# Kernel tuning notes

Hardware: AMD Instinct MI355X
Metric: run time of the kernel (lower is better)

The kernel has to match this reference:

```python
import jax, jax.numpy as jnp
import numpy as np

XMIN, XMAX = -16.0, 16.0
ZMIN, ZMAX = -16.0, 16.0
SOFTCLIP_L = 5.0


def ref2mem(traj, Zs, Xs):
    # traj: (B, T, 2) cam (x, z) -> mem pixel coords
    x = (traj[..., 0] - XMIN) / ((XMAX - XMIN) / Xs) - 0.5
    z = (traj[..., 1] - ZMIN) / ((ZMAX - ZMIN) / Zs) - 0.5
    return x, z


def bilinear_sample2d(pm, x, z):
    # pm: (B, C, Z, X); x, z: (B, N) float coords -> (B, C, N)
    B, C, Zs, Xs = pm.shape
    x = jnp.clip(x, 0.0, Xs - 1.0)
    z = jnp.clip(z, 0.0, Zs - 1.0)
    x0 = jnp.floor(x).astype(jnp.int32)
    z0 = jnp.floor(z).astype(jnp.int32)
    x1 = jnp.minimum(x0 + 1, Xs - 1)
    z1 = jnp.minimum(z0 + 1, Zs - 1)
    wx = x - x0.astype(x.dtype)
    wz = z - z0.astype(z.dtype)
    pm_flat = pm.reshape(B, C, Zs * Xs)

    def gather(zi, xi):
        idx = (zi * Xs + xi)[:, None, :]  # (B,1,N)
        return jnp.take_along_axis(pm_flat, jnp.broadcast_to(idx, (B, C, idx.shape[-1])), axis=2)

    v00 = gather(z0, x0); v01 = gather(z0, x1)
    v10 = gather(z1, x0); v11 = gather(z1, x1)
    wx = wx[:, None, :]; wz = wz[:, None, :]
    return (v00 * (1 - wx) * (1 - wz) + v01 * wx * (1 - wz)
            + v10 * (1 - wx) * wz + v11 * wx * wz)


def gru_cell(x, h, W_ih, W_hh, b_ih, b_hh):
    gi = x @ W_ih.T + b_ih
    gh = h @ W_hh.T + b_hh
    i_r, i_z, i_n = jnp.split(gi, 3, axis=1)
    h_r, h_z, h_n = jnp.split(gh, 3, axis=1)
    r = jax.nn.sigmoid(i_r + h_r)
    z = jax.nn.sigmoid(i_z + h_z)
    n = jnp.tanh(i_n + r * h_n)
    return (1.0 - z) * n + z * h


def expm_softclip(sig_raw):
    B = sig_raw.shape[0]
    nrm = jnp.linalg.norm(sig_raw.reshape(B, -1), axis=1)
    denom = jax.nn.logsumexp(jnp.stack([nrm / SOFTCLIP_L, jnp.ones_like(nrm)], axis=-1), axis=-1)
    return sig_raw / denom[:, None, None]


def reference(feat_map, pred_map, noise, traj_past,
              W_ih, W_hh, b_ih, b_hh, past_W, past_b,
              W1, b1, W2, b2, W3, b3):
    B, C, Zf, Xf = feat_map.shape
    Zp, Xp = pred_map.shape[2], pred_map.shape[3]
    T_futu = noise.shape[1]
    H = W_hh.shape[1]
    eye2 = jnp.eye(2, dtype=feat_map.dtype)

    # static feature: max_pool2d k=8 s=8 + past encoding
    pooled = feat_map.reshape(B, C, Zf // 8, 8, Xf // 8, 8).max(axis=(3, 5)).reshape(B, -1)
    past_enc = traj_past.reshape(B, -1) @ past_W.T + past_b
    sta_feat = jnp.concatenate([pooled, past_enc], axis=1)  # (B, 2080)

    def step(carry, noise_t):
        hx, win = carry
        xm, zm = ref2mem(win, Zp, Xp)
        feats = bilinear_sample2d(pred_map, xm, zm).reshape(B, -1)  # (B, 3)
        dyn_feat = jnp.concatenate([feats, win.reshape(B, -1)], axis=1)  # (B, 9)
        hx = gru_cell(dyn_feat, hx, W_ih, W_hh, b_ih, b_hh)
        joint = jnp.concatenate([hx, sta_feat], axis=1)  # (B, 2112)
        h1 = jax.nn.leaky_relu(joint @ W1.T + b1)
        h2 = jax.nn.leaky_relu(h1 @ W2.T + b2)
        pred = h2 @ W3.T + b3  # (B, 6)
        mu = pred[:, :2]
        sig_raw = pred[:, 2:].reshape(B, 2, 2) + 1e-8 * eye2
        sig_raw = expm_softclip(sig_raw)
        sig = jnp.einsum('bij,bkj->bik', sig_raw, sig_raw)
        xdotdot = mu + jnp.sum(sig * noise_t[:, None, :], axis=1)
        x_next = 2.0 * win[:, -1] - win[:, -2] + xdotdot  # verlet, dt=1
        win = jnp.concatenate([win[:, 1:], x_next[:, None]], axis=1)
        return (hx, win), x_next

    hx0 = jnp.zeros((B, H), dtype=feat_map.dtype)
    (_, _), traj_futu = jax.lax.scan(step, (hx0, traj_past), jnp.swapaxes(noise, 0, 1))
    return jnp.swapaxes(traj_futu, 0, 1)  # (B, T_futu, 2)


def setup_inputs():
    key = jax.random.key(0)
    ks = jax.random.split(key, 16)
    B, C, Zf, Xf = 192, 32, 64, 64
    T_futu, T_past, H = 27, 3, 32
    d = {}
    d['feat_map'] = jax.random.normal(ks[0], (B, C, Zf, Xf), jnp.float32)
    d['pred_map'] = jax.random.normal(ks[1], (B, 1, Zf, Xf), jnp.float32)
    d['noise'] = jax.random.normal(ks[2], (B, T_futu, 2), jnp.float32)
    d['traj_past'] = jax.random.normal(ks[3], (B, T_past, 2), jnp.float32) * 4.0
    s = 0.05
    d['W_ih'] = jax.random.normal(ks[4], (3 * H, 9), jnp.float32) * s
    d['W_hh'] = jax.random.normal(ks[5], (3 * H, H), jnp.float32) * s
    d['b_ih'] = jnp.zeros((3 * H,), jnp.float32)
    d['b_hh'] = jnp.zeros((3 * H,), jnp.float32)
    d['past_W'] = jax.random.normal(ks[6], (32, T_past * 2), jnp.float32) * s
    d['past_b'] = jnp.zeros((32,), jnp.float32)
    d['W1'] = jax.random.normal(ks[7], (64, 2112), jnp.float32) * 0.02
    d['b1'] = jnp.zeros((64,), jnp.float32)
    d['W2'] = jax.random.normal(ks[8], (32, 64), jnp.float32) * s
    d['b2'] = jnp.zeros((32,), jnp.float32)
    d['W3'] = jax.random.normal(ks[9], (6, 32), jnp.float32) * s
    d['b3'] = jnp.zeros((6,), jnp.float32)
    return d
```

## Files before the change

kernel.cpp:

```cpp
#include <hip/hip_runtime.h>
#include <hip/hip_bf16.h>
#include <math.h>

typedef unsigned int u32;
typedef __fp16 f16x2 __attribute__((ext_vector_type(2)));
typedef u32 u32x4 __attribute__((ext_vector_type(4)));

#define NB    192
#define NC    32
#define TFUT  27
#define BLOB_F_OFF (NB * 64)

#if __has_builtin(__builtin_amdgcn_rcpf)
#define RCPF(x) __builtin_amdgcn_rcpf(x)
#else
#define RCPF(x) (1.0f / (x))
#endif
#if __has_builtin(__builtin_amdgcn_sqrtf)
#define SQRTF(x) __builtin_amdgcn_sqrtf(x)
#else
#define SQRTF(x) sqrtf(x)
#endif
#if __has_builtin(__builtin_amdgcn_exp2f)
#define EXP2F(x) __builtin_amdgcn_exp2f(x)
#else
#define EXP2F(x) exp2f(x)
#endif
#if __has_builtin(__builtin_amdgcn_logf)
#define LOG2F(x) __builtin_amdgcn_logf(x)
#else
#define LOG2F(x) log2f(x)
#endif

__device__ __forceinline__ u32 pk16(float lo, float hi) {
    auto v = __builtin_amdgcn_cvt_pkrtz(lo, hi);
    return __builtin_bit_cast(u32, v);
}
__device__ __forceinline__ float fdot2pk(u32 a, u32 b, float c) {
#if __has_builtin(__builtin_amdgcn_fdot2)
    return __builtin_amdgcn_fdot2(__builtin_bit_cast(f16x2, a),
                                  __builtin_bit_cast(f16x2, b), c, false);
#else
    f16x2 av = __builtin_bit_cast(f16x2, a), bv = __builtin_bit_cast(f16x2, b);
    return c + (float)av[0] * (float)bv[0] + (float)av[1] * (float)bv[1];
#endif
}
__device__ __forceinline__ u32 rdl(u32 v, int lane) {
    return (u32)__builtin_amdgcn_readlane((int)v, lane);
}
__device__ __forceinline__ float rdlf(float v, int lane) {
    return __int_as_float(__builtin_amdgcn_readlane(__float_as_int(v), lane));
}
__device__ __forceinline__ float dpp_xor1(float v) {
    return __int_as_float(__builtin_amdgcn_update_dpp(
        0, __float_as_int(v), 0xB1, 0xF, 0xF, true));
}
__device__ __forceinline__ float perm32hi(float v) {
    int x = __float_as_int(v), y = x;
    asm volatile("v_permlane32_swap_b32 %0, %1" : "+v"(x), "+v"(y));
    return __int_as_float(x);
}
__device__ __forceinline__ float sigmoid_f(float x) {
    return RCPF(1.0f + EXP2F(-1.4426950408889634f * x));
}
__device__ __forceinline__ float tanh_f(float x) {
    return __builtin_fmaf(2.0f, RCPF(1.0f + EXP2F(-2.8853900817779268f * x)), -1.0f);
}

__global__ __launch_bounds__(1024) void k_static(
    const float* __restrict__ feat,
    const float* __restrict__ traj_past,
    const float* __restrict__ past_W,
    const float* __restrict__ past_b,
    const float* __restrict__ W1,
    const float* __restrict__ b1,
    const float* __restrict__ W_ih,
    const float* __restrict__ W_hh,
    const float* __restrict__ b_ih,
    const float* __restrict__ b_hh,
    const float* __restrict__ W2,
    const float* __restrict__ b2,
    const float* __restrict__ W3,
    const float* __restrict__ b3,
    float* __restrict__ ws)
{
    const int b = blockIdx.x;
    const int t = threadIdx.x;

    if (b == NB) {
        if (t >= 64) return;
        const int l = t, m2 = l & 31;
        u32* blob = reinterpret_cast<u32*>(ws) + BLOB_F_OFF + (size_t)l * 128;
        #pragma unroll
        for (int k = 0; k < 9; ++k) {
            blob[k]     = __float_as_uint(W_ih[l * 9 + k]);
            blob[9 + k] = __float_as_uint(W_ih[(64 + m2) * 9 + k]);
        }
        #pragma unroll
        for (int j = 0; j < 16; ++j) {
            blob[18 + j] = pk16(W_hh[l * 32 + 2*j],          W_hh[l * 32 + 2*j + 1]);
            blob[34 + j] = pk16(W_hh[(64 + m2) * 32 + 2*j],  W_hh[(64 + m2) * 32 + 2*j + 1]);
            blob[50 + j] = pk16(W1[(size_t)l * 2112 + 2*j],  W1[(size_t)l * 2112 + 2*j + 1]);
        }
        #pragma unroll
        for (int j = 0; j < 32; ++j)
            blob[66 + j] = pk16(W2[m2 * 64 + 2*j], W2[m2 * 64 + 2*j + 1]);
        const int wr = (l < 6) ? l : 0;
        #pragma unroll
        for (int j = 0; j < 16; ++j)
            blob[98 + j] = pk16(W3[wr * 32 + 2*j], W3[wr * 32 + 2*j + 1]);
        blob[114] = __float_as_uint(b_ih[l]);
        blob[115] = __float_as_uint(b_hh[l]);
        blob[116] = __float_as_uint(b_ih[64 + m2]);
        blob[117] = __float_as_uint(b_hh[64 + m2]);
        blob[118] = __float_as_uint(b2[m2]);
        #pragma unroll
        for (int r = 0; r < 6; ++r) blob[119 + r] = __float_as_uint(b3[r]);
        blob[125] = blob[126] = blob[127] = 0u;
        return;
    }

    __shared__ __align__(16) float sta[2080];

    for (int it = 0; it < 2; ++it) {
        const int c    = it * 16 + (t >> 6);
        const int cell = t & 63;
        const int zi = cell >> 3, xi = cell & 7;
        const float* p = feat + ((size_t)b * NC + c) * 4096 + zi * 8 * 64 + xi * 8;
        float m = -3.402823466e38f;
        #pragma unroll
        for (int dz = 0; dz < 8; ++dz) {
            const float4 v0 = *reinterpret_cast<const float4*>(p + dz * 64);
            const float4 v1 = *reinterpret_cast<const float4*>(p + dz * 64 + 4);
            m = fmaxf(m, fmaxf(fmaxf(fmaxf(v0.x, v0.y), fmaxf(v0.z, v0.w)),
                               fmaxf(fmaxf(v1.x, v1.y), fmaxf(v1.z, v1.w))));
        }
        sta[c * 64 + cell] = m;
    }
    if (t < 32) {
        float acc = past_b[t];
        #pragma unroll
        for (int k = 0; k < 6; ++k) acc += past_W[t * 6 + k] * traj_past[b * 6 + k];
        sta[2048 + t] = acc;
    }
    __syncthreads();

    const int o = t >> 4, l = t & 15;
    const float* wrow = W1 + (size_t)o * 2112 + 32;
    float acc = 0.f;
    #pragma unroll 4
    for (int j = 0; j < 32; ++j) {
        const int k = j * 64 + l * 4;
        const float4 w = *reinterpret_cast<const float4*>(wrow + k);
        const float4 s = *reinterpret_cast<const float4*>(&sta[k]);
        acc += w.x * s.x + w.y * s.y + w.z * s.z + w.w * s.w;
    }
    if (l < 8) {
        const int k = 2048 + l * 4;
        const float4 w = *reinterpret_cast<const float4*>(wrow + k);
        const float4 s = *reinterpret_cast<const float4*>(&sta[k]);
        acc += w.x * s.x + w.y * s.y + w.z * s.z + w.w * s.w;
    }
    acc += __shfl_xor(acc, 1);
    acc += __shfl_xor(acc, 2);
    acc += __shfl_xor(acc, 4);
    acc += __shfl_xor(acc, 8);
    if (l == 0) ws[b * 64 + o] = b1[o] + acc;
}

__global__ __launch_bounds__(64, 1) void k_recur(
    const float* __restrict__ pred_map,
    const float* __restrict__ noise,
    const float* __restrict__ traj_past,
    const float* __restrict__ ws,
    float* __restrict__ out)
{
    __shared__ __align__(16) float pm[4096];

    const int b = blockIdx.x;
    const int l = threadIdx.x;

    {
        const float4* src = reinterpret_cast<const float4*>(pred_map + (size_t)b * 4096);
        float4* dst = reinterpret_cast<float4*>(pm);
        #pragma unroll
        for (int i = 0; i < 16; ++i) dst[l + i * 64] = src[l + i * 64];
    }
    const float nzreg = (l < TFUT * 2) ? noise[b * (TFUT * 2) + l] : 0.f;

    const u32* blob = reinterpret_cast<const u32*>(ws) + BLOB_F_OFF + (size_t)l * 128;
    u32x4 dv[32];
    #pragma unroll
    for (int j = 0; j < 32; ++j)
        dv[j] = reinterpret_cast<const u32x4*>(blob)[j];
#define DW(i) (dv[(i) >> 2][(i) & 3])
#define DF(i) __int_as_float((int)DW(i))

    const float sta1l = ws[b * 64 + l];

    float w[6];
    #pragma unroll
    for (int j = 0; j < 6; ++j) w[j] = traj_past[b * 6 + j];
    float hxp = 0.f;
    u32 hxpk[16];
    #pragma unroll
    for (int j = 0; j < 16; ++j) hxpk[j] = 0u;
    float Adot = 0.f, Cdot = 0.f;

    __syncthreads();

    auto bsamp = [&](float px, float pz) -> float {
        float x = (px + 16.0f) * 2.0f - 0.5f;
        float z = (pz + 16.0f) * 2.0f - 0.5f;
        x = fminf(fmaxf(x, 0.0f), 63.0f);
        z = fminf(fmaxf(z, 0.0f), 63.0f);
        const float xf = floorf(x), zf = floorf(z);
        const int x0 = (int)xf, z0 = (int)zf;
        const int x1 = min(x0 + 1, 63), z1 = min(z0 + 1, 63);
        const float wx = x - xf, wz = z - zf;
        const float v00 = pm[z0 * 64 + x0], v01 = pm[z0 * 64 + x1];
        const float v10 = pm[z1 * 64 + x0], v11 = pm[z1 * 64 + x1];
        return v00 * (1.f - wx) * (1.f - wz) + v01 * wx * (1.f - wz)
             + v10 * (1.f - wx) * wz        + v11 * wx * wz;
    };
    float sm0 = bsamp(w[0], w[1]);
    float sm1 = bsamp(w[2], w[3]);
    float sm2 = bsamp(w[4], w[5]);

    for (int ts = 0; ts < TFUT; ++ts) {
        float gi  = DF(114) + DF(3) * w[0] + DF(4) * w[1] + DF(5) * w[2]
                            + DF(6) * w[3] + DF(7) * w[4] + DF(8) * w[5];
        float gi2 = DF(116) + DF(12) * w[0] + DF(13) * w[1] + DF(14) * w[2]
                            + DF(15) * w[3] + DF(16) * w[4] + DF(17) * w[5];
        gi  += DF(0) * sm0 + DF(1) * sm1 + DF(2) * sm2;
        gi2 += DF(9) * sm0 + DF(10) * sm1 + DF(11) * sm2;

        const float gs = gi + DF(115) + Adot;
        const float sg = sigmoid_f(gs);
        const float zv = perm32hi(sg);
        const float nv = tanh_f(gi2 + sg * (DF(117) + Cdot));
        const float hn = (1.0f - zv) * nv + zv * hxp;
        hxp = hn;

        const u32 hpk = pk16(hn, dpp_xor1(hn));
        #pragma unroll
        for (int j = 0; j < 16; ++j) hxpk[j] = rdl(hpk, 2 * j);

        float D0 = 0.f, D1 = 0.f, D2 = 0.f, D3 = 0.f;
        #pragma unroll
        for (int j = 0; j < 16; j += 4) {
            D0 = fdot2pk(hxpk[j],   DW(50 + j),     D0);
            D1 = fdot2pk(hxpk[j+1], DW(50 + j + 1), D1);
            D2 = fdot2pk(hxpk[j+2], DW(50 + j + 2), D2);
            D3 = fdot2pk(hxpk[j+3], DW(50 + j + 3), D3);
        }
        const float h1a = sta1l + ((D0 + D1) + (D2 + D3));
        const float h1l = (h1a >= 0.f) ? h1a : 0.01f * h1a;

        const u32 h1p = pk16(h1l, dpp_xor1(h1l));
        u32 h1pk[32];
        #pragma unroll
        for (int j = 0; j < 32; ++j) h1pk[j] = rdl(h1p, 2 * j);

        float P0 = 0.f, P1 = 0.f, P2 = 0.f, P3 = 0.f;
        float P4 = 0.f, P5 = 0.f, P6 = 0.f, P7 = 0.f;
        #pragma unroll
        for (int j = 0; j < 32; j += 8) {
            P0 = fdot2pk(h1pk[j],   DW(66 + j),     P0);
            P1 = fdot2pk(h1pk[j+1], DW(66 + j + 1), P1);
            P2 = fdot2pk(h1pk[j+2], DW(66 + j + 2), P2);
            P3 = fdot2pk(h1pk[j+3], DW(66 + j + 3), P3);
            P4 = fdot2pk(h1pk[j+4], DW(66 + j + 4), P4);
            P5 = fdot2pk(h1pk[j+5], DW(66 + j + 5), P5);
            P6 = fdot2pk(h1pk[j+6], DW(66 + j + 6), P6);
            P7 = fdot2pk(h1pk[j+7], DW(66 + j + 7), P7);
        }
        const float h2a = DF(118) + (((P0 + P1) + (P2 + P3)) + ((P4 + P5) + (P6 + P7)));
        const float h2l = (h2a >= 0.f) ? h2a : 0.01f * h2a;

        const u32 h2p = pk16(h2l, dpp_xor1(h2l));
        u32 h2pk[16];
        #pragma unroll
        for (int j = 0; j < 16; ++j) h2pk[j] = rdl(h2p, 2 * j);

        float Q0 = 0.f, Q1 = 0.f, Q2 = 0.f, Q3 = 0.f;
        #pragma unroll
        for (int j = 0; j < 16; j += 4) {
            Q0 = fdot2pk(h2pk[j],   DW(98 + j),     Q0);
            Q1 = fdot2pk(h2pk[j+1], DW(98 + j + 1), Q1);
            Q2 = fdot2pk(h2pk[j+2], DW(98 + j + 2), Q2);
            Q3 = fdot2pk(h2pk[j+3], DW(98 + j + 3), Q3);
        }
        const float praw = (Q0 + Q1) + (Q2 + Q3);

        const float pv0 = rdlf(praw, 0) + DF(119);
        const float pv1 = rdlf(praw, 1) + DF(120);
        const float pv2 = rdlf(praw, 2) + DF(121);
        const float pv3 = rdlf(praw, 3) + DF(122);
        const float pv4 = rdlf(praw, 4) + DF(123);
        const float pv5 = rdlf(praw, 5) + DF(124);

        const float s00 = pv2 + 1e-8f, s01 = pv3;
        const float s10 = pv4,          s11 = pv5 + 1e-8f;
        const float p00 = s00 * s00 + s01 * s01;
        const float p01 = s00 * s10 + s01 * s11;
        const float p11 = s10 * s10 + s11 * s11;
        const float nrm = SQRTF(p00 + p11);
        const float arg = nrm * 0.2f;
        const float mmx = fmaxf(arg, 1.0f);
        const float dd  = fabsf(arg - 1.0f);
        const float den = mmx + 0.6931471805599453f *
                          LOG2F(1.0f + EXP2F(-1.4426950408889634f * dd));
        const float inv  = RCPF(den);
        const float inv2 = inv * inv;

        const float nnx = rdlf(nzreg, 2 * ts);
        const float nny = rdlf(nzreg, 2 * ts + 1);
        const float xd0 = pv0 + nnx * ((p00 + p01) * inv2);
        const float xd1 = pv1 + nny * ((p01 + p11) * inv2);
        const float nx0 = 2.0f * w[4] - w[2] + xd0;
        const float nx1 = 2.0f * w[5] - w[3] + xd1;

        if (l == 0) {
            float2 o; o.x = nx0; o.y = nx1;
            *reinterpret_cast<float2*>(out + ((size_t)b * TFUT + ts) * 2) = o;
        }

        w[0] = w[2]; w[1] = w[3];
        w[2] = w[4]; w[3] = w[5];
        w[4] = nx0;  w[5] = nx1;
        sm0 = sm1; sm1 = sm2;

        float v00, v01, v10, v11, wxs, wzs;
        {
            float x = (nx0 + 16.0f) * 2.0f - 0.5f;
            float z = (nx1 + 16.0f) * 2.0f - 0.5f;
            x = fminf(fmaxf(x, 0.0f), 63.0f);
            z = fminf(fmaxf(z, 0.0f), 63.0f);
            const float xf = floorf(x), zf = floorf(z);
            const int x0 = (int)xf, z0 = (int)zf;
            const int x1 = min(x0 + 1, 63), z1 = min(z0 + 1, 63);
            wxs = x - xf; wzs = z - zf;
            v00 = pm[z0 * 64 + x0]; v01 = pm[z0 * 64 + x1];
            v10 = pm[z1 * 64 + x0]; v11 = pm[z1 * 64 + x1];
        }

        {
            float A0 = 0.f, A1 = 0.f, A2 = 0.f, A3 = 0.f;
            float C0 = 0.f, C1 = 0.f, C2 = 0.f, C3 = 0.f;
            #pragma unroll
            for (int j = 0; j < 16; j += 4) {
                A0 = fdot2pk(hxpk[j],   DW(18 + j),     A0);
                A1 = fdot2pk(hxpk[j+1], DW(18 + j + 1), A1);
                A2 = fdot2pk(hxpk[j+2], DW(18 + j + 2), A2);
                A3 = fdot2pk(hxpk[j+3], DW(18 + j + 3), A3);
                C0 = fdot2pk(hxpk[j],   DW(34 + j),     C0);
                C1 = fdot2pk(hxpk[j+1], DW(34 + j + 1), C1);
                C2 = fdot2pk(hxpk[j+2], DW(34 + j + 2), C2);
                C3 = fdot2pk(hxpk[j+3], DW(34 + j + 3), C3);
            }
            Adot = (A0 + A1) + (A2 + A3);
            Cdot = (C0 + C1) + (C2 + C3);
        }

        sm2 = v00 * (1.f - wxs) * (1.f - wzs) + v01 * wxs * (1.f - wzs)
            + v10 * (1.f - wxs) * wzs        + v11 * wxs * wzs;
    }
#undef DW
#undef DF
}

extern "C" void kernel_launch(void* const* d_in, const int* in_sizes, int n_in,
                              void* d_out, int out_size, void* d_ws, size_t ws_size,
                              hipStream_t stream) {
    const float* feat      = (const float*)d_in[0];
    const float* pred_map  = (const float*)d_in[1];
    const float* noise     = (const float*)d_in[2];
    const float* traj_past = (const float*)d_in[3];
    const float* W_ih      = (const float*)d_in[4];
    const float* W_hh      = (const float*)d_in[5];
    const float* b_ih      = (const float*)d_in[6];
    const float* b_hh      = (const float*)d_in[7];
    const float* past_W    = (const float*)d_in[8];
    const float* past_b    = (const float*)d_in[9];
    const float* W1        = (const float*)d_in[10];
    const float* b1        = (const float*)d_in[11];
    const float* W2        = (const float*)d_in[12];
    const float* b2        = (const float*)d_in[13];
    const float* W3        = (const float*)d_in[14];
    const float* b3        = (const float*)d_in[15];
    float* outp = (float*)d_out;
    float* ws   = (float*)d_ws;

    k_static<<<dim3(NB + 1), dim3(1024), 0, stream>>>(
        feat, traj_past, past_W, past_b, W1, b1,
        W_ih, W_hh, b_ih, b_hh, W2, b2, W3, b3, ws);
    k_recur<<<dim3(NB), dim3(64), 0, stream>>>(pred_map, noise, traj_past, ws, outp);
}
```

Before: 45.91 us.

## Broadcast recurrent vectors through LDS and split MLP dot products across half-waves

The per-step broadcasts of packed hidden vectors now go through small shared-memory buffers read back with vector loads, replacing long chains of readlane instructions. The W2 and W3 dot products are split so each half-wave covers half the inputs, and the halves are combined with a permlane32 swap, which shrinks the register weight blob. The A and C GRU dot products are moved earlier in the step to overlap with the MLP chain, and the bilinear sample uses lerp form. This relies on single-wave execution and only a compiler fence for LDS ordering, which is fragile. The perm32hi return value was also changed.

```diff
diff --git a/kernel.cpp b/kernel.cpp
--- a/kernel.cpp
+++ b/kernel.cpp
@@ -32,6 +32,8 @@
 #define LOG2F(x) log2f(x)
 #endif
 
+#define LDS_FENCE() asm volatile("" ::: "memory")
+
 __device__ __forceinline__ u32 pk16(float lo, float hi) {
     auto v = __builtin_amdgcn_cvt_pkrtz(lo, hi);
     return __builtin_bit_cast(u32, v);
@@ -45,9 +47,6 @@
     return c + (float)av[0] * (float)bv[0] + (float)av[1] * (float)bv[1];
 #endif
 }
-__device__ __forceinline__ u32 rdl(u32 v, int lane) {
-    return (u32)__builtin_amdgcn_readlane((int)v, lane);
-}
 __device__ __forceinline__ float rdlf(float v, int lane) {
     return __int_as_float(__builtin_amdgcn_readlane(__float_as_int(v), lane));
 }
@@ -58,7 +57,7 @@
 __device__ __forceinline__ float perm32hi(float v) {
     int x = __float_as_int(v), y = x;
     asm volatile("v_permlane32_swap_b32 %0, %1" : "+v"(x), "+v"(y));
-    return __int_as_float(x);
+    return __int_as_float(y);
 }
 __device__ __forceinline__ float sigmoid_f(float x) {
     return RCPF(1.0f + EXP2F(-1.4426950408889634f * x));
@@ -89,7 +88,7 @@
 
     if (b == NB) {
         if (t >= 64) return;
-        const int l = t, m2 = l & 31;
+        const int l = t, m2 = l & 31, h = l >> 5;
         u32* blob = reinterpret_cast<u32*>(ws) + BLOB_F_OFF + (size_t)l * 128;
         #pragma unroll
         for (int k = 0; k < 9; ++k) {
@@ -103,20 +102,20 @@
             blob[50 + j] = pk16(W1[(size_t)l * 2112 + 2*j],  W1[(size_t)l * 2112 + 2*j + 1]);
         }
         #pragma unroll
-        for (int j = 0; j < 32; ++j)
-            blob[66 + j] = pk16(W2[m2 * 64 + 2*j], W2[m2 * 64 + 2*j + 1]);
-        const int wr = (l < 6) ? l : 0;
-        #pragma unroll
         for (int j = 0; j < 16; ++j)
-            blob[98 + j] = pk16(W3[wr * 32 + 2*j], W3[wr * 32 + 2*j + 1]);
-        blob[114] = __float_as_uint(b_ih[l]);
-        blob[115] = __float_as_uint(b_hh[l]);
-        blob[116] = __float_as_uint(b_ih[64 + m2]);
-        blob[117] = __float_as_uint(b_hh[64 + m2]);
-        blob[118] = __float_as_uint(b2[m2]);
-        #pragma unroll
-        for (int r = 0; r < 6; ++r) blob[119 + r] = __float_as_uint(b3[r]);
-        blob[125] = blob[126] = blob[127] = 0u;
+            blob[66 + j] = pk16(W2[m2 * 64 + h * 32 + 2*j], W2[m2 * 64 + h * 32 + 2*j + 1]);
+        const int wr = (m2 < 6) ? m2 : 0;
+        #pragma unroll
+        for (int j = 0; j < 8; ++j)
+            blob[82 + j] = pk16(W3[wr * 32 + h * 16 + 2*j], W3[wr * 32 + h * 16 + 2*j + 1]);
+        blob[90] = __float_as_uint(b_ih[l]);
+        blob[91] = __float_as_uint(b_hh[l]);
+        blob[92] = __float_as_uint(b_ih[64 + m2]);
+        blob[93] = __float_as_uint(b_hh[64 + m2]);
+        blob[94] = __float_as_uint(b2[m2]);
+        #pragma unroll
+        for (int r = 0; r < 6; ++r) blob[95 + r] = __float_as_uint(b3[r]);
+        blob[101] = blob[102] = blob[103] = 0u;
         return;
     }
 
@@ -176,9 +175,14 @@
     float* __restrict__ out)
 {
     __shared__ __align__(16) float pm[4096];
+    __shared__ __align__(16) u32 hxbw[32];
+    __shared__ __align__(16) u32 h1bw[32];
+    __shared__ __align__(16) u32 h2bw[32];
 
     const int b = blockIdx.x;
     const int l = threadIdx.x;
+    const int h = l >> 5;
+    const bool odd = (l & 1);
 
     {
         const float4* src = reinterpret_cast<const float4*>(pred_map + (size_t)b * 4096);
@@ -189,9 +193,9 @@
     const float nzreg = (l < TFUT * 2) ? noise[b * (TFUT * 2) + l] : 0.f;
 
     const u32* blob = reinterpret_cast<const u32*>(ws) + BLOB_F_OFF + (size_t)l * 128;
-    u32x4 dv[32];
+    u32x4 dv[26];
     #pragma unroll
-    for (int j = 0; j < 32; ++j)
+    for (int j = 0; j < 26; ++j)
         dv[j] = reinterpret_cast<const u32x4*>(blob)[j];
 #define DW(i) (dv[(i) >> 2][(i) & 3])
 #define DF(i) __int_as_float((int)DW(i))
@@ -202,16 +206,13 @@
     #pragma unroll
     for (int j = 0; j < 6; ++j) w[j] = traj_past[b * 6 + j];
     float hxp = 0.f;
-    u32 hxpk[16];
-    #pragma unroll
-    for (int j = 0; j < 16; ++j) hxpk[j] = 0u;
     float Adot = 0.f, Cdot = 0.f;
 
     __syncthreads();
 
     auto bsamp = [&](float px, float pz) -> float {
-        float x = (px + 16.0f) * 2.0f - 0.5f;
-        float z = (pz + 16.0f) * 2.0f - 0.5f;
+        float x = __builtin_fmaf(2.0f, px, 31.5f);
+        float z = __builtin_fmaf(2.0f, pz, 31.5f);
         x = fminf(fmaxf(x, 0.0f), 63.0f);
         z = fminf(fmaxf(z, 0.0f), 63.0f);
         const float xf = floorf(x), zf = floorf(z);
@@ -220,85 +221,140 @@
         const float wx = x - xf, wz = z - zf;
         const float v00 = pm[z0 * 64 + x0], v01 = pm[z0 * 64 + x1];
         const float v10 = pm[z1 * 64 + x0], v11 = pm[z1 * 64 + x1];
-        return v00 * (1.f - wx) * (1.f - wz) + v01 * wx * (1.f - wz)
-             + v10 * (1.f - wx) * wz        + v11 * wx * wz;
+        const float top = v00 + wx * (v01 - v00);
+        const float bot = v10 + wx * (v11 - v10);
+        return top + wz * (bot - top);
     };
     float sm0 = bsamp(w[0], w[1]);
     float sm1 = bsamp(w[2], w[3]);
     float sm2 = bsamp(w[4], w[5]);
 
+    auto pkpair = [&](float v) -> u32 {
+        const float nb = dpp_xor1(v);
+        const float plo = odd ? nb : v;
+        const float phi = odd ? v : nb;
+        return pk16(plo, phi);
+    };
+
     for (int ts = 0; ts < TFUT; ++ts) {
-        float gi  = DF(114) + DF(3) * w[0] + DF(4) * w[1] + DF(5) * w[2]
-                            + DF(6) * w[3] + DF(7) * w[4] + DF(8) * w[5];
-        float gi2 = DF(116) + DF(12) * w[0] + DF(13) * w[1] + DF(14) * w[2]
-                            + DF(15) * w[3] + DF(16) * w[4] + DF(17) * w[5];
-        gi  += DF(0) * sm0 + DF(1) * sm1 + DF(2) * sm2;
-        gi2 += DF(9) * sm0 + DF(10) * sm1 + DF(11) * sm2;
-
-        const float gs = gi + DF(115) + Adot;
+        float giA = DF(90) + DF(3) * w[0] + DF(4) * w[1];
+        float giB = DF(5) * w[2] + DF(6) * w[3];
+        float giC = DF(7) * w[4] + DF(8) * w[5];
+        float giD = DF(0) * sm0 + DF(1) * sm1 + DF(2) * sm2;
+        const float gi = (giA + giB) + (giC + giD);
+
+        float gjA = DF(92) + DF(12) * w[0] + DF(13) * w[1];
+        float gjB = DF(14) * w[2] + DF(15) * w[3];
+        float gjC = DF(16) * w[4] + DF(17) * w[5];
+        float gjD = DF(9) * sm0 + DF(10) * sm1 + DF(11) * sm2;
+        const float gi2 = (gjA + gjB) + (gjC + gjD);
+
+        const float gs = gi + DF(91) + Adot;
         const float sg = sigmoid_f(gs);
         const float zv = perm32hi(sg);
-        const float nv = tanh_f(gi2 + sg * (DF(117) + Cdot));
+        const float nv = tanh_f(gi2 + sg * (DF(93) + Cdot));
         const float hn = (1.0f - zv) * nv + zv * hxp;
         hxp = hn;
 
-        const u32 hpk = pk16(hn, dpp_xor1(hn));
-        #pragma unroll
-        for (int j = 0; j < 16; ++j) hxpk[j] = rdl(hpk, 2 * j);
+        hxbw[l >> 1] = pkpair(hn);
+        LDS_FENCE();
+        u32 hxpk[16];
+        {
+            const u32x4* r = reinterpret_cast<const u32x4*>(hxbw);
+            const u32x4 t0 = r[0], t1 = r[1], t2 = r[2], t3 = r[3];
+            #pragma unroll
+            for (int q = 0; q < 4; ++q) {
+                hxpk[q]      = t0[q];
+                hxpk[4 + q]  = t1[q];
+                hxpk[8 + q]  = t2[q];
+                hxpk[12 + q] = t3[q];
+            }
+        }
 
         float D0 = 0.f, D1 = 0.f, D2 = 0.f, D3 = 0.f;
+        float A0 = 0.f, A1 = 0.f, A2 = 0.f, A3 = 0.f;
         #pragma unroll
         for (int j = 0; j < 16; j += 4) {
             D0 = fdot2pk(hxpk[j],   DW(50 + j),     D0);
             D1 = fdot2pk(hxpk[j+1], DW(50 + j + 1), D1);
             D2 = fdot2pk(hxpk[j+2], DW(50 + j + 2), D2);
             D3 = fdot2pk(hxpk[j+3], DW(50 + j + 3), D3);
-        }
+            A0 = fdot2pk(hxpk[j],   DW(18 + j),     A0);
+            A1 = fdot2pk(hxpk[j+1], DW(18 + j + 1), A1);
+            A2 = fdot2pk(hxpk[j+2], DW(18 + j + 2), A2);
+            A3 = fdot2pk(hxpk[j+3], DW(18 + j + 3), A3);
+        }
+        Adot = (A0 + A1) + (A2 + A3);
         const float h1a = sta1l + ((D0 + D1) + (D2 + D3));
         const float h1l = (h1a >= 0.f) ? h1a : 0.01f * h1a;
 
-        const u32 h1p = pk16(h1l, dpp_xor1(h1l));
-        u32 h1pk[32];
-        #pragma unroll
-        for (int j = 0; j < 32; ++j) h1pk[j] = rdl(h1p, 2 * j);
+        h1bw[l >> 1] = pkpair(h1l);
+        LDS_FENCE();
+        u32 h1in[16];
+        {
+            const u32x4* r = reinterpret_cast<const u32x4*>(h1bw + (h << 4));
+            const u32x4 t0 = r[0], t1 = r[1], t2 = r[2], t3 = r[3];
+            #pragma unroll
+            for (int q = 0; q < 4; ++q) {
+                h1in[q]      = t0[q];
+                h1in[4 + q]  = t1[q];
+                h1in[8 + q]  = t2[q];
+                h1in[12 + q] = t3[q];
+            }
+        }
+
+        float C0 = 0.f, C1 = 0.f, C2 = 0.f, C3 = 0.f;
+        #pragma unroll
+        for (int j = 0; j < 16; j += 4) {
+            C0 = fdot2pk(hxpk[j],   DW(34 + j),     C0);
+            C1 = fdot2pk(hxpk[j+1], DW(34 + j + 1), C1);
+            C2 = fdot2pk(hxpk[j+2], DW(34 + j + 2), C2);
+            C3 = fdot2pk(hxpk[j+3], DW(34 + j + 3), C3);
+        }
+        Cdot = (C0 + C1) + (C2 + C3);
 
         float P0 = 0.f, P1 = 0.f, P2 = 0.f, P3 = 0.f;
-        float P4 = 0.f, P5 = 0.f, P6 = 0.f, P7 = 0.f;
-        #pragma unroll
-        for (int j = 0; j < 32; j += 8) {
-            P0 = fdot2pk(h1pk[j],   DW(66 + j),     P0);
-            P1 = fdot2pk(h1pk[j+1], DW(66 + j + 1), P1);
-            P2 = fdot2pk(h1pk[j+2], DW(66 + j + 2), P2);
-            P3 = fdot2pk(h1pk[j+3], DW(66 + j + 3), P3);
-            P4 = fdot2pk(h1pk[j+4], DW(66 + j + 4), P4);
-            P5 = fdot2pk(h1pk[j+5], DW(66 + j + 5), P5);
-            P6 = fdot2pk(h1pk[j+6], DW(66 + j + 6), P6);
-            P7 = fdot2pk(h1pk[j+7], DW(66 + j + 7), P7);
-        }
-        const float h2a = DF(118) + (((P0 + P1) + (P2 + P3)) + ((P4 + P5) + (P6 + P7)));
+        #pragma unroll
+        for (int j = 0; j < 16; j += 4) {
+            P0 = fdot2pk(h1in[j],   DW(66 + j),     P0);
+            P1 = fdot2pk(h1in[j+1], DW(66 + j + 1), P1);
+            P2 = fdot2pk(h1in[j+2], DW(66 + j + 2), P2);
+            P3 = fdot2pk(h1in[j+3], DW(66 + j + 3), P3);
+        }
+        const float Pown = (P0 + P1) + (P2 + P3);
+        const float h2a = DF(94) + Pown + perm32hi(Pown);
         const float h2l = (h2a >= 0.f) ? h2a : 0.01f * h2a;
 
-        const u32 h2p = pk16(h2l, dpp_xor1(h2l));
-        u32 h2pk[16];
-        #pragma unroll
-        for (int j = 0; j < 16; ++j) h2pk[j] = rdl(h2p, 2 * j);
+        h2bw[l >> 1] = pkpair(h2l);
+        LDS_FENCE();
+        u32 h2in[8];
+        {
+            const u32x4* r = reinterpret_cast<const u32x4*>(h2bw + (h << 3));
+            const u32x4 t0 = r[0], t1 = r[1];
+            #pragma unroll
+            for (int q = 0; q < 4; ++q) {
+                h2in[q]     = t0[q];
+                h2in[4 + q] = t1[q];
+            }
+        }
 
         float Q0 = 0.f, Q1 = 0.f, Q2 = 0.f, Q3 = 0.f;
         #pragma unroll
-        for (int j = 0; j < 16; j += 4) {
-            Q0 = fdot2pk(h2pk[j],   DW(98 + j),     Q0);
-            Q1 = fdot2pk(h2pk[j+1], DW(98 + j + 1), Q1);
-            Q2 = fdot2pk(h2pk[j+2], DW(98 + j + 2), Q2);
-            Q3 = fdot2pk(h2pk[j+3], DW(98 + j + 3), Q3);
-        }
-        const float praw = (Q0 + Q1) + (Q2 + Q3);
-
-        const float pv0 = rdlf(praw, 0) + DF(119);
-        const float pv1 = rdlf(praw, 1) + DF(120);
-        const float pv2 = rdlf(praw, 2) + DF(121);
-        const float pv3 = rdlf(praw, 3) + DF(122);
-        const float pv4 = rdlf(praw, 4) + DF(123);
-        const float pv5 = rdlf(praw, 5) + DF(124);
+        for (int j = 0; j < 8; j += 4) {
+            Q0 = fdot2pk(h2in[j],   DW(82 + j),     Q0);
+            Q1 = fdot2pk(h2in[j+1], DW(82 + j + 1), Q1);
+            Q2 = fdot2pk(h2in[j+2], DW(82 + j + 2), Q2);
+            Q3 = fdot2pk(h2in[j+3], DW(82 + j + 3), Q3);
+        }
+        const float Qown = (Q0 + Q1) + (Q2 + Q3);
+        const float praw = Qown + perm32hi(Qown);
+
+        const float pv0 = rdlf(praw, 0) + DF(95);
+        const float pv1 = rdlf(praw, 1) + DF(96);
+        const float pv2 = rdlf(praw, 2) + DF(97);
+        const float pv3 = rdlf(praw, 3) + DF(98);
+        const float pv4 = rdlf(praw, 4) + DF(99);
+        const float pv5 = rdlf(praw, 5) + DF(100);
 
         const float s00 = pv2 + 1e-8f, s01 = pv3;
         const float s10 = pv4,          s11 = pv5 + 1e-8f;
@@ -330,41 +386,7 @@
         w[2] = w[4]; w[3] = w[5];
         w[4] = nx0;  w[5] = nx1;
         sm0 = sm1; sm1 = sm2;
-
-        float v00, v01, v10, v11, wxs, wzs;
-        {
-            float x = (nx0 + 16.0f) * 2.0f - 0.5f;
-            float z = (nx1 + 16.0f) * 2.0f - 0.5f;
-            x = fminf(fmaxf(x, 0.0f), 63.0f);
-            z = fminf(fmaxf(z, 0.0f), 63.0f);
-            const float xf = floorf(x), zf = floorf(z);
-            const int x0 = (int)xf, z0 = (int)zf;
-            const int x1 = min(x0 + 1, 63), z1 = min(z0 + 1, 63);
-            wxs = x - xf; wzs = z - zf;
-            v00 = pm[z0 * 64 + x0]; v01 = pm[z0 * 64 + x1];
-            v10 = pm[z1 * 64 + x0]; v11 = pm[z1 * 64 + x1];
-        }
-
-        {
-            float A0 = 0.f, A1 = 0.f, A2 = 0.f, A3 = 0.f;
-            float C0 = 0.f, C1 = 0.f, C2 = 0.f, C3 = 0.f;
-            #pragma unroll
-            for (int j = 0; j < 16; j += 4) {
-                A0 = fdot2pk(hxpk[j],   DW(18 + j),     A0);
-                A1 = fdot2pk(hxpk[j+1], DW(18 + j + 1), A1);
-                A2 = fdot2pk(hxpk[j+2], DW(18 + j + 2), A2);
-                A3 = fdot2pk(hxpk[j+3], DW(18 + j + 3), A3);
-                C0 = fdot2pk(hxpk[j],   DW(34 + j),     C0);
-                C1 = fdot2pk(hxpk[j+1], DW(34 + j + 1), C1);
-                C2 = fdot2pk(hxpk[j+2], DW(34 + j + 2), C2);
-                C3 = fdot2pk(hxpk[j+3], DW(34 + j + 3), C3);
-            }
-            Adot = (A0 + A1) + (A2 + A3);
-            Cdot = (C0 + C1) + (C2 + C3);
-        }
-
-        sm2 = v00 * (1.f - wxs) * (1.f - wzs) + v01 * wxs * (1.f - wzs)
-            + v10 * (1.f - wxs) * wzs        + v11 * wxs * wzs;
+        sm2 = bsamp(nx0, nx1);
     }
 #undef DW
 #undef DF
```

After: 44.63 us. -2.8%, faster.
